# Kernel optimization log

Measured on AMD Instinct MI355X. Metric: run time of the kernel, lower is better.

The kernel has to match this reference:

```python
import jax, jax.numpy as jnp
import numpy as np

N, E, C, L, OUT = 50000, 600000, 128, 2, 64


def setup_inputs() -> dict:
    key = jax.random.key(0)
    ks = jax.random.split(key, 8)
    s = 1.0 / np.sqrt(C)
    return {
        "x": jax.random.normal(ks[0], (N, C), jnp.float32),
        "edge_index": jax.random.randint(ks[1], (2, E), 0, N, jnp.int64),
        "W_neigh": jax.random.normal(ks[2], (L, C, C), jnp.float32) * s,
        "W_root": jax.random.normal(ks[3], (L, C, C), jnp.float32) * s,
        "b_conv": jnp.zeros((L, C), jnp.float32),
        "ln_gamma": jnp.ones((L, C), jnp.float32),
        "ln_beta": jnp.zeros((L, C), jnp.float32),
        "W_head": jax.random.normal(ks[4], (OUT, C), jnp.float32) * s,
        "b_head": jnp.zeros((OUT,), jnp.float32),
        "num_seed": 1024,
    }


def _layernorm(h, g, b, eps=1e-5):
    mu = jnp.mean(h, axis=-1, keepdims=True)
    var = jnp.mean(jnp.square(h - mu), axis=-1, keepdims=True)
    return (h - mu) * jax.lax.rsqrt(var + eps) * g + b


def reference(x, edge_index, W_neigh, W_root, b_conv, ln_gamma, ln_beta, W_head, b_head, num_seed):
    src, dst = edge_index[0], edge_index[1]
    n = x.shape[0]
    # in-degree for mean aggregation (clamped to 1 as in PyG mean aggr)
    deg = jax.ops.segment_sum(jnp.ones((src.shape[0],), x.dtype), dst, num_segments=n)
    inv_deg = 1.0 / jnp.maximum(deg, 1.0)  # [N]
    for l in range(W_neigh.shape[0]):
        agg = jax.ops.segment_sum(x[src], dst, num_segments=n) * inv_deg[:, None]  # [N,C]
        h = agg @ W_neigh[l].T + x @ W_root[l].T + b_conv[l]
        x = jax.nn.relu(_layernorm(h, ln_gamma[l], ln_beta[l]))
    # head on the seed nodes (entity table slice starts at 0 here)
    return x[:num_seed] @ W_head.T + b_head
```

## Files before the change

### kernel.cpp

```cpp
#include <hip/hip_runtime.h>

#define C 128

typedef __attribute__((ext_vector_type(8))) short short8;
typedef __attribute__((ext_vector_type(16))) float floatx16;

__device__ __forceinline__ unsigned short f2b(float f) {
    union { float f; unsigned u; } v; v.f = f;
    unsigned u = v.u + 0x7fffu + ((v.u >> 16) & 1u);
    return (unsigned short)(u >> 16);
}
__device__ __forceinline__ void acc_pair(unsigned u, float& lo, float& hi) {
    union { unsigned u; float f; } a, b;
    a.u = u << 16;
    b.u = u & 0xffff0000u;
    lo += a.f;
    hi += b.f;
}

__global__ void cast_mark_count_kernel(const float* __restrict__ x, unsigned short* __restrict__ xb, int n4x,
                                       const float* __restrict__ Wn, unsigned short* __restrict__ Wnb,
                                       const float* __restrict__ Wr, unsigned short* __restrict__ Wrb, int n4w,
                                       const float* __restrict__ Wh, unsigned short* __restrict__ Whb, int n4h,
                                       const int* __restrict__ src, const int* __restrict__ dst,
                                       int* __restrict__ deg, int* __restrict__ needed,
                                       int E, int num_seed,
                                       int castBlocks) {
    if ((int)blockIdx.x < castBlocks) {
        int i = blockIdx.x * blockDim.x + threadIdx.x;
        const float* in;
        unsigned short* out;
        int idx;
        if (i < n4x) { in = x; out = xb; idx = i; }
        else if (i < n4x + n4w) { in = Wn; out = Wnb; idx = i - n4x; }
        else if (i < n4x + 2 * n4w) { in = Wr; out = Wrb; idx = i - n4x - n4w; }
        else if (i < n4x + 2 * n4w + n4h) { in = Wh; out = Whb; idx = i - n4x - 2 * n4w; }
        else return;
        float4 v = ((const float4*)in)[idx];
        ushort4 o;
        o.x = f2b(v.x); o.y = f2b(v.y); o.z = f2b(v.z); o.w = f2b(v.w);
        ((ushort4*)out)[idx] = o;
    } else {
        int e = (blockIdx.x - castBlocks) * blockDim.x + threadIdx.x;
        if (e < num_seed) needed[e] = 1;
        if (e < E) {
            int d = dst[e];
            atomicAdd(&deg[d], 1);
            if (d < num_seed) needed[src[e]] = 1;
        }
    }
}

__global__ void scan_fused_kernel(const int* __restrict__ deg, const int* __restrict__ needed,
                                  unsigned long long* __restrict__ status, int* __restrict__ counter,
                                  int* __restrict__ row_start, int* __restrict__ cursor,
                                  int* __restrict__ nodelist, int* __restrict__ Mptr, int n) {
    __shared__ int smD[256];
    __shared__ int smN[256];
    __shared__ int sbid, sprefD, sprefN;
    int t = threadIdx.x;
    if (t == 0) sbid = atomicAdd(counter, 1);
    __syncthreads();
    int bid = sbid;
    int i = bid * 256 + t;
    int d = (i < n) ? deg[i] : 0;
    int nd = (i < n) ? needed[i] : 0;
    smD[t] = d; smN[t] = nd;
    __syncthreads();
    for (int off = 1; off < 256; off <<= 1) {
        int vD = (t >= off) ? smD[t - off] : 0;
        int vN = (t >= off) ? smN[t - off] : 0;
        __syncthreads();
        smD[t] += vD; smN[t] += vN;
        __syncthreads();
    }
    int totD = smD[255], totN = smN[255];
    if (t == 0) {
        if (bid == 0) {
            atomicExch(&status[0],
                       (2ULL << 62) | ((unsigned long long)(unsigned)totN << 32) | (unsigned)totD);
            sprefD = 0; sprefN = 0;
        } else {
            atomicExch(&status[bid],
                       (1ULL << 62) | ((unsigned long long)(unsigned)totN << 32) | (unsigned)totD);
            int accD = 0, accN = 0;
            for (int j = bid - 1; j >= 0;) {
                unsigned long long v = atomicAdd(&status[j], 0ULL);
                unsigned f = (unsigned)(v >> 62);
                if (f == 0) { __builtin_amdgcn_s_sleep(1); continue; }
                accD += (int)(unsigned)(v & 0xffffffffULL);
                accN += (int)((v >> 32) & 0x3fffffffULL);
                if (f == 2) break;
                --j;
            }
            atomicExch(&status[bid],
                       (2ULL << 62) | ((unsigned long long)(unsigned)(accN + totN) << 32) |
                           (unsigned)(accD + totD));
            sprefD = accD; sprefN = accN;
        }
    }
    __syncthreads();
    int exD = smD[t] - d + sprefD;
    int exN = smN[t] - nd + sprefN;
    if (i < n) {
        row_start[i] = exD;
        cursor[i] = exD;
        if (nd) nodelist[exN] = i;
        if (i == n - 1) { row_start[n] = exD + d; *Mptr = exN + nd; }
    }
}

__global__ void bucket_kernel(const int* __restrict__ src, const int* __restrict__ dst,
                              int* __restrict__ cursor, int* __restrict__ esrc, int E,
                              const int* __restrict__ needed) {
    int e = blockIdx.x * blockDim.x + threadIdx.x;
    if (e < E) {
        int d = dst[e];
        if (needed[d]) {
            int p = atomicAdd(&cursor[d], 1);
            esrc[p] = src[e];
        }
    }
}

__launch_bounds__(256)
__global__ void gemm_fused_kernel(const unsigned short* __restrict__ cur,
                                  const int* __restrict__ row_start, const int* __restrict__ esrc,
                                  const unsigned short* __restrict__ Wn,
                                  const unsigned short* __restrict__ Wr,
                                  const float* __restrict__ bconv, const float* __restrict__ gamma,
                                  const float* __restrict__ beta, unsigned short* __restrict__ Xout,
                                  int n,
                                  const int* __restrict__ nodelist, const int* __restrict__ Mptr,
                                  const unsigned short* __restrict__ Whb,
                                  const float* __restrict__ bh, float* __restrict__ out) {
    __shared__ unsigned short Xs[64][136];
    __shared__ unsigned short Ws[128][136];
    __shared__ float Ls[64][2];
    __shared__ float Lss[64][2];

    int m = Mptr ? *Mptr : n;
    int row0 = blockIdx.x * 64;
    if (row0 >= m) return;

    int tid = threadIdx.x;
    int wave = tid >> 6, lane = tid & 63;
    int rh = wave & 1, ch = wave >> 1;
    int l31 = lane & 31, half = lane >> 5;

#pragma unroll
    for (int i = 0; i < 8; ++i) {
        int cidx = tid + 256 * i;
        int r = cidx >> 4, koff = (cidx & 15) * 8;
        *(uint4*)&Ws[r][koff] = *(const uint4*)(Wn + (size_t)r * C + koff);
    }

    int q = lane >> 4, l16 = lane & 15, qb = lane & 48;
    size_t choff = (size_t)l16 * 8;
#pragma unroll
    for (int pass = 0; pass < 4; ++pass) {
        int rl = pass * 16 + wave * 4 + q;
        int rg = row0 + rl;
        float a0 = 0.f, a1 = 0.f, a2 = 0.f, a3 = 0.f, a4 = 0.f, a5 = 0.f, a6 = 0.f, a7 = 0.f;
        float sc = 0.f;
        if (rg < m) {
            int node = nodelist ? nodelist[rg] : rg;
            int beg = row_start[node];
            int end = row_start[node + 1];
            for (int base = beg; base < end; base += 16) {
                int cnt = min(end - base, 16);
                int e_val = (base + l16 < end) ? esrc[base + l16] : 0;
                int j = 0;
                for (; j + 8 <= cnt; j += 8) {
                    int s0 = __shfl(e_val, qb | j, 64);
                    int s1 = __shfl(e_val, qb | (j + 1), 64);
                    int s2 = __shfl(e_val, qb | (j + 2), 64);
                    int s3 = __shfl(e_val, qb | (j + 3), 64);
                    int s4 = __shfl(e_val, qb | (j + 4), 64);
                    int s5 = __shfl(e_val, qb | (j + 5), 64);
                    int s6 = __shfl(e_val, qb | (j + 6), 64);
                    int s7 = __shfl(e_val, qb | (j + 7), 64);
                    uint4 v0 = *(const uint4*)(cur + (size_t)s0 * C + choff);
                    uint4 v1 = *(const uint4*)(cur + (size_t)s1 * C + choff);
                    uint4 v2 = *(const uint4*)(cur + (size_t)s2 * C + choff);
                    uint4 v3 = *(const uint4*)(cur + (size_t)s3 * C + choff);
                    uint4 v4 = *(const uint4*)(cur + (size_t)s4 * C + choff);
                    uint4 v5 = *(const uint4*)(cur + (size_t)s5 * C + choff);
                    uint4 v6 = *(const uint4*)(cur + (size_t)s6 * C + choff);
                    uint4 v7 = *(const uint4*)(cur + (size_t)s7 * C + choff);
                    acc_pair(v0.x, a0, a1); acc_pair(v0.y, a2, a3); acc_pair(v0.z, a4, a5); acc_pair(v0.w, a6, a7);
                    acc_pair(v1.x, a0, a1); acc_pair(v1.y, a2, a3); acc_pair(v1.z, a4, a5); acc_pair(v1.w, a6, a7);
                    acc_pair(v2.x, a0, a1); acc_pair(v2.y, a2, a3); acc_pair(v2.z, a4, a5); acc_pair(v2.w, a6, a7);
                    acc_pair(v3.x, a0, a1); acc_pair(v3.y, a2, a3); acc_pair(v3.z, a4, a5); acc_pair(v3.w, a6, a7);
                    acc_pair(v4.x, a0, a1); acc_pair(v4.y, a2, a3); acc_pair(v4.z, a4, a5); acc_pair(v4.w, a6, a7);
                    acc_pair(v5.x, a0, a1); acc_pair(v5.y, a2, a3); acc_pair(v5.z, a4, a5); acc_pair(v5.w, a6, a7);
                    acc_pair(v6.x, a0, a1); acc_pair(v6.y, a2, a3); acc_pair(v6.z, a4, a5); acc_pair(v6.w, a6, a7);
                    acc_pair(v7.x, a0, a1); acc_pair(v7.y, a2, a3); acc_pair(v7.z, a4, a5); acc_pair(v7.w, a6, a7);
                }
                for (; j + 4 <= cnt; j += 4) {
                    int s0 = __shfl(e_val, qb | j, 64);
                    int s1 = __shfl(e_val, qb | (j + 1), 64);
                    int s2 = __shfl(e_val, qb | (j + 2), 64);
                    int s3 = __shfl(e_val, qb | (j + 3), 64);
                    uint4 v0 = *(const uint4*)(cur + (size_t)s0 * C + choff);
                    uint4 v1 = *(const uint4*)(cur + (size_t)s1 * C + choff);
                    uint4 v2 = *(const uint4*)(cur + (size_t)s2 * C + choff);
                    uint4 v3 = *(const uint4*)(cur + (size_t)s3 * C + choff);
                    acc_pair(v0.x, a0, a1); acc_pair(v0.y, a2, a3); acc_pair(v0.z, a4, a5); acc_pair(v0.w, a6, a7);
                    acc_pair(v1.x, a0, a1); acc_pair(v1.y, a2, a3); acc_pair(v1.z, a4, a5); acc_pair(v1.w, a6, a7);
                    acc_pair(v2.x, a0, a1); acc_pair(v2.y, a2, a3); acc_pair(v2.z, a4, a5); acc_pair(v2.w, a6, a7);
                    acc_pair(v3.x, a0, a1); acc_pair(v3.y, a2, a3); acc_pair(v3.z, a4, a5); acc_pair(v3.w, a6, a7);
                }
                for (; j < cnt; ++j) {
                    int s0 = __shfl(e_val, qb | j, 64);
                    uint4 v0 = *(const uint4*)(cur + (size_t)s0 * C + choff);
                    acc_pair(v0.x, a0, a1); acc_pair(v0.y, a2, a3); acc_pair(v0.z, a4, a5); acc_pair(v0.w, a6, a7);
                }
            }
            sc = 1.0f / fmaxf((float)(end - beg), 1.0f);
        }
        uint4 o;
        o.x = ((unsigned)f2b(a1 * sc) << 16) | (unsigned)f2b(a0 * sc);
        o.y = ((unsigned)f2b(a3 * sc) << 16) | (unsigned)f2b(a2 * sc);
        o.z = ((unsigned)f2b(a5 * sc) << 16) | (unsigned)f2b(a4 * sc);
        o.w = ((unsigned)f2b(a7 * sc) << 16) | (unsigned)f2b(a6 * sc);
        *(uint4*)&Xs[rl][choff] = o;
    }
    __syncthreads();

    floatx16 acc0, acc1;
#pragma unroll
    for (int i = 0; i < 16; ++i) { acc0[i] = 0.f; acc1[i] = 0.f; }

#pragma unroll
    for (int kc = 0; kc < C; kc += 16) {
        int ko = kc + half * 8;
        short8 a = *(const short8*)&Xs[rh * 32 + l31][ko];
        short8 b0 = *(const short8*)&Ws[ch * 64 + l31][ko];
        short8 b1 = *(const short8*)&Ws[ch * 64 + 32 + l31][ko];
        acc0 = __builtin_amdgcn_mfma_f32_32x32x16_bf16(a, b0, acc0, 0, 0, 0);
        acc1 = __builtin_amdgcn_mfma_f32_32x32x16_bf16(a, b1, acc1, 0, 0, 0);
    }
    __syncthreads();

#pragma unroll
    for (int i = 0; i < 4; ++i) {
        int cidx = tid + 256 * i;
        int r = cidx >> 4, koff = (cidx & 15) * 8;
        uint4 v = make_uint4(0u, 0u, 0u, 0u);
        int rg = row0 + r;
        if (rg < m) {
            int rowid = nodelist ? nodelist[rg] : rg;
            v = *(const uint4*)(cur + (size_t)rowid * C + koff);
        }
        *(uint4*)&Xs[r][koff] = v;
    }
#pragma unroll
    for (int i = 0; i < 8; ++i) {
        int cidx = tid + 256 * i;
        int r = cidx >> 4, koff = (cidx & 15) * 8;
        *(uint4*)&Ws[r][koff] = *(const uint4*)(Wr + (size_t)r * C + koff);
    }
    __syncthreads();

#pragma unroll
    for (int kc = 0; kc < C; kc += 16) {
        int ko = kc + half * 8;
        short8 a = *(const short8*)&Xs[rh * 32 + l31][ko];
        short8 b0 = *(const short8*)&Ws[ch * 64 + l31][ko];
        short8 b1 = *(const short8*)&Ws[ch * 64 + 32 + l31][ko];
        acc0 = __builtin_amdgcn_mfma_f32_32x32x16_bf16(a, b0, acc0, 0, 0, 0);
        acc1 = __builtin_amdgcn_mfma_f32_32x32x16_bf16(a, b1, acc1, 0, 0, 0);
    }

    int col0 = ch * 64 + l31;
    int col1 = col0 + 32;
    float bc0 = bconv[col0], bc1 = bconv[col1];
#pragma unroll
    for (int r = 0; r < 16; ++r) {
        float h0 = acc0[r] + bc0;
        float h1 = acc1[r] + bc1;
        float s = h0 + h1, ss = h0 * h0 + h1 * h1;
#pragma unroll
        for (int mk = 1; mk < 32; mk <<= 1) {
            s += __shfl_xor(s, mk, 64);
            ss += __shfl_xor(ss, mk, 64);
        }
        if (l31 == 0) {
            int row_l = rh * 32 + (r & 3) + 8 * (r >> 2) + 4 * half;
            Ls[row_l][ch] = s;
            Lss[row_l][ch] = ss;
        }
    }
    __syncthreads();

    if (Whb) {
#pragma unroll
        for (int i = 0; i < 4; ++i) {
            int cidx = tid + 256 * i;
            int r = cidx >> 4, koff = (cidx & 15) * 8;
            uint4 v = *(const uint4*)(Whb + (size_t)r * C + koff);
            *(uint4*)&Ws[r][koff] = v;
        }
    }

    float g0 = gamma[col0], g1 = gamma[col1];
    float be0 = beta[col0], be1 = beta[col1];
#pragma unroll
    for (int r = 0; r < 16; ++r) {
        int row_l = rh * 32 + (r & 3) + 8 * (r >> 2) + 4 * half;
        int rg = row0 + row_l;
        float s = Ls[row_l][0] + Ls[row_l][1];
        float ss = Lss[row_l][0] + Lss[row_l][1];
        float mu = s * (1.0f / 128.0f);
        float var = ss * (1.0f / 128.0f) - mu * mu;
        float rs = rsqrtf(var + 1e-5f);
        float h0 = acc0[r] + bc0;
        float h1 = acc1[r] + bc1;
        float o0 = fmaxf((h0 - mu) * rs * g0 + be0, 0.f);
        float o1 = fmaxf((h1 - mu) * rs * g1 + be1, 0.f);
        if (Whb) {
            Xs[row_l][col0] = f2b(o0);
            Xs[row_l][col1] = f2b(o1);
        } else if (rg < m) {
            int orow = nodelist ? nodelist[rg] : rg;
            Xout[(size_t)orow * C + col0] = f2b(o0);
            Xout[(size_t)orow * C + col1] = f2b(o1);
        }
    }

    if (Whb) {
        __syncthreads();
        floatx16 hc;
#pragma unroll
        for (int i = 0; i < 16; ++i) hc[i] = 0.f;
        int m0 = rh * 32, n0 = ch * 32;
#pragma unroll
        for (int kc = 0; kc < C; kc += 16) {
            int ko = kc + half * 8;
            short8 a = *(const short8*)&Xs[m0 + l31][ko];
            short8 b = *(const short8*)&Ws[n0 + l31][ko];
            hc = __builtin_amdgcn_mfma_f32_32x32x16_bf16(a, b, hc, 0, 0, 0);
        }
        int oc = n0 + l31;
        float bhv = bh[oc];
#pragma unroll
        for (int r = 0; r < 16; ++r) {
            int row_l = m0 + (r & 3) + 8 * (r >> 2) + 4 * half;
            int rg = row0 + row_l;
            if (rg < m) out[(size_t)rg * 64 + oc] = hc[r] + bhv;
        }
    }
}

extern "C" void kernel_launch(void* const* d_in, const int* in_sizes, int n_in,
                              void* d_out, int out_size, void* d_ws, size_t ws_size,
                              hipStream_t stream) {
    const float* x = (const float*)d_in[0];
    const int* ei = (const int*)d_in[1];
    const float* Wn = (const float*)d_in[2];
    const float* Wr = (const float*)d_in[3];
    const float* bconv = (const float*)d_in[4];
    const float* gamma = (const float*)d_in[5];
    const float* beta = (const float*)d_in[6];
    const float* Wh = (const float*)d_in[7];
    const float* bh = (const float*)d_in[8];

    int N = in_sizes[0] / C;
    int E = in_sizes[1] / 2;
    int L = in_sizes[2] / (C * C);
    int num_seed = out_size / 64;
    int nchunks = (N + 255) / 256;

    char* ws = (char*)d_ws;
    size_t off = 0;
    auto alloc = [&](size_t bytes) {
        void* p = ws + off;
        off = (off + bytes + 255) & ~(size_t)255;
        return p;
    };
    int* deg = (int*)alloc((size_t)N * 4);
    int* needed = (int*)alloc((size_t)N * 4);
    int* counter = (int*)alloc(256);
    unsigned long long* status = (unsigned long long*)alloc((size_t)nchunks * 8);
    size_t zero_span = off;
    int* row_start = (int*)alloc((size_t)(N + 1) * 4);
    int* cursor = (int*)alloc((size_t)N * 4);
    int* nodelist = (int*)alloc((size_t)N * 4);
    int* Mptr = (int*)alloc(4);
    int* esrc = (int*)alloc((size_t)E * 4);
    unsigned short* xb = (unsigned short*)alloc((size_t)N * C * 2);
    unsigned short* xA = (unsigned short*)alloc((size_t)N * C * 2);
    unsigned short* xB = (unsigned short*)alloc((size_t)N * C * 2);
    unsigned short* Wnb = (unsigned short*)alloc((size_t)L * C * C * 2);
    unsigned short* Wrb = (unsigned short*)alloc((size_t)L * C * C * 2);
    unsigned short* Whb = (unsigned short*)alloc((size_t)64 * C * 2);

    const int* srcIdx = ei;
    const int* dstIdx = ei + E;

    int n4x = N * C / 4;
    int n4w = L * C * C / 4;
    int n4h = 64 * C / 4;
    int castBlocks = (n4x + 2 * n4w + n4h + 255) / 256;
    int degBlocks = (max(E, num_seed) + 255) / 256;

    hipMemsetAsync(ws, 0, zero_span, stream);
    cast_mark_count_kernel<<<castBlocks + degBlocks, 256, 0, stream>>>(
        x, xb, n4x, Wn, Wnb, Wr, Wrb, n4w, Wh, Whb, n4h,
        srcIdx, dstIdx, deg, needed, E, num_seed, castBlocks);
    scan_fused_kernel<<<nchunks, 256, 0, stream>>>(deg, needed, status, counter,
                                                   row_start, cursor, nodelist, Mptr, N);
    bucket_kernel<<<(E + 255) / 256, 256, 0, stream>>>(srcIdx, dstIdx, cursor, esrc, E, needed);

    const unsigned short* cur = xb;
    unsigned short* bufs[2] = {xA, xB};
    for (int l = 0; l < L; ++l) {
        bool last = (l == L - 1);
        bool front = !last && (l == L - 2);
        int nl = last ? num_seed : N;
        const int* list = front ? nodelist : nullptr;
        const int* Mp = front ? Mptr : nullptr;
        unsigned short* nxt = bufs[l & 1];
        gemm_fused_kernel<<<(nl + 63) / 64, 256, 0, stream>>>(
            cur, row_start, esrc,
            Wnb + (size_t)l * C * C, Wrb + (size_t)l * C * C,
            bconv + (size_t)l * C, gamma + (size_t)l * C, beta + (size_t)l * C, nxt, nl,
            list, Mp,
            last ? Whb : (const unsigned short*)nullptr, bh, (float*)d_out);
        cur = nxt;
    }
}
```

Measured before the change: 197.9 us.

## Split neighbor aggregation into a separate kernel before the MFMA GEMM

Moves the gather-and-mean neighbor aggregation out of the fused GEMM kernel into its own wave-per-four-nodes kernel, which writes a bf16 aggregate buffer. The GEMM kernel then loads the aggregate and root rows into shared memory in a uniform two-phase loop and stages its output in LDS for coalesced uint4 stores. The aim is higher occupancy and better latency hiding for the irregular gather, and a simpler, lighter GEMM kernel. The cost is an extra launch per layer plus a write and re-read of an N×C bf16 intermediate.

```diff
diff --git a/kernel.cpp b/kernel.cpp
--- a/kernel.cpp
+++ b/kernel.cpp
@@ -123,17 +123,96 @@
     }
 }
 
+__global__ void aggregate_kernel(const unsigned short* __restrict__ xb, const int* __restrict__ row_start,
+                                 const int* __restrict__ esrc,
+                                 unsigned short* __restrict__ agg, int n,
+                                 const int* __restrict__ nodelist, const int* __restrict__ Mptr) {
+    int wid = (blockIdx.x * blockDim.x + threadIdx.x) >> 6;
+    int lane = threadIdx.x & 63;
+    int q = lane >> 4, l16 = lane & 15;
+    int qb = lane & 48;
+    int pos = wid * 4 + q;
+    int m = Mptr ? *Mptr : n;
+    if (pos >= m) return;
+    int node = nodelist ? nodelist[pos] : pos;
+
+    int beg = row_start[node];
+    int end = row_start[node + 1];
+    size_t choff = (size_t)l16 * 8;
+
+    float a0 = 0.f, a1 = 0.f, a2 = 0.f, a3 = 0.f, a4 = 0.f, a5 = 0.f, a6 = 0.f, a7 = 0.f;
+
+    for (int base = beg; base < end; base += 16) {
+        int cnt = min(end - base, 16);
+        int e_val = (base + l16 < end) ? esrc[base + l16] : 0;
+        int j = 0;
+        for (; j + 8 <= cnt; j += 8) {
+            int s0 = __shfl(e_val, qb | j, 64);
+            int s1 = __shfl(e_val, qb | (j + 1), 64);
+            int s2 = __shfl(e_val, qb | (j + 2), 64);
+            int s3 = __shfl(e_val, qb | (j + 3), 64);
+            int s4 = __shfl(e_val, qb | (j + 4), 64);
+            int s5 = __shfl(e_val, qb | (j + 5), 64);
+            int s6 = __shfl(e_val, qb | (j + 6), 64);
+            int s7 = __shfl(e_val, qb | (j + 7), 64);
+            uint4 v0 = *(const uint4*)(xb + (size_t)s0 * C + choff);
+            uint4 v1 = *(const uint4*)(xb + (size_t)s1 * C + choff);
+            uint4 v2 = *(const uint4*)(xb + (size_t)s2 * C + choff);
+            uint4 v3 = *(const uint4*)(xb + (size_t)s3 * C + choff);
+            uint4 v4 = *(const uint4*)(xb + (size_t)s4 * C + choff);
+            uint4 v5 = *(const uint4*)(xb + (size_t)s5 * C + choff);
+            uint4 v6 = *(const uint4*)(xb + (size_t)s6 * C + choff);
+            uint4 v7 = *(const uint4*)(xb + (size_t)s7 * C + choff);
+            acc_pair(v0.x, a0, a1); acc_pair(v0.y, a2, a3); acc_pair(v0.z, a4, a5); acc_pair(v0.w, a6, a7);
+            acc_pair(v1.x, a0, a1); acc_pair(v1.y, a2, a3); acc_pair(v1.z, a4, a5); acc_pair(v1.w, a6, a7);
+            acc_pair(v2.x, a0, a1); acc_pair(v2.y, a2, a3); acc_pair(v2.z, a4, a5); acc_pair(v2.w, a6, a7);
+            acc_pair(v3.x, a0, a1); acc_pair(v3.y, a2, a3); acc_pair(v3.z, a4, a5); acc_pair(v3.w, a6, a7);
+            acc_pair(v4.x, a0, a1); acc_pair(v4.y, a2, a3); acc_pair(v4.z, a4, a5); acc_pair(v4.w, a6, a7);
+            acc_pair(v5.x, a0, a1); acc_pair(v5.y, a2, a3); acc_pair(v5.z, a4, a5); acc_pair(v5.w, a6, a7);
+            acc_pair(v6.x, a0, a1); acc_pair(v6.y, a2, a3); acc_pair(v6.z, a4, a5); acc_pair(v6.w, a6, a7);
+            acc_pair(v7.x, a0, a1); acc_pair(v7.y, a2, a3); acc_pair(v7.z, a4, a5); acc_pair(v7.w, a6, a7);
+        }
+        for (; j + 4 <= cnt; j += 4) {
+            int s0 = __shfl(e_val, qb | j, 64);
+            int s1 = __shfl(e_val, qb | (j + 1), 64);
+            int s2 = __shfl(e_val, qb | (j + 2), 64);
+            int s3 = __shfl(e_val, qb | (j + 3), 64);
+            uint4 v0 = *(const uint4*)(xb + (size_t)s0 * C + choff);
+            uint4 v1 = *(const uint4*)(xb + (size_t)s1 * C + choff);
+            uint4 v2 = *(const uint4*)(xb + (size_t)s2 * C + choff);
+            uint4 v3 = *(const uint4*)(xb + (size_t)s3 * C + choff);
+            acc_pair(v0.x, a0, a1); acc_pair(v0.y, a2, a3); acc_pair(v0.z, a4, a5); acc_pair(v0.w, a6, a7);
+            acc_pair(v1.x, a0, a1); acc_pair(v1.y, a2, a3); acc_pair(v1.z, a4, a5); acc_pair(v1.w, a6, a7);
+            acc_pair(v2.x, a0, a1); acc_pair(v2.y, a2, a3); acc_pair(v2.z, a4, a5); acc_pair(v2.w, a6, a7);
+            acc_pair(v3.x, a0, a1); acc_pair(v3.y, a2, a3); acc_pair(v3.z, a4, a5); acc_pair(v3.w, a6, a7);
+        }
+        for (; j < cnt; ++j) {
+            int s0 = __shfl(e_val, qb | j, 64);
+            uint4 v0 = *(const uint4*)(xb + (size_t)s0 * C + choff);
+            acc_pair(v0.x, a0, a1); acc_pair(v0.y, a2, a3); acc_pair(v0.z, a4, a5); acc_pair(v0.w, a6, a7);
+        }
+    }
+
+    float sc = 1.0f / fmaxf((float)(end - beg), 1.0f);
+    uint4 o;
+    o.x = ((unsigned)f2b(a1 * sc) << 16) | (unsigned)f2b(a0 * sc);
+    o.y = ((unsigned)f2b(a3 * sc) << 16) | (unsigned)f2b(a2 * sc);
+    o.z = ((unsigned)f2b(a5 * sc) << 16) | (unsigned)f2b(a4 * sc);
+    o.w = ((unsigned)f2b(a7 * sc) << 16) | (unsigned)f2b(a6 * sc);
+    *(uint4*)(agg + (size_t)pos * C + choff) = o;
+}
+
 __launch_bounds__(256)
-__global__ void gemm_fused_kernel(const unsigned short* __restrict__ cur,
-                                  const int* __restrict__ row_start, const int* __restrict__ esrc,
-                                  const unsigned short* __restrict__ Wn,
-                                  const unsigned short* __restrict__ Wr,
-                                  const float* __restrict__ bconv, const float* __restrict__ gamma,
-                                  const float* __restrict__ beta, unsigned short* __restrict__ Xout,
-                                  int n,
-                                  const int* __restrict__ nodelist, const int* __restrict__ Mptr,
-                                  const unsigned short* __restrict__ Whb,
-                                  const float* __restrict__ bh, float* __restrict__ out) {
+__global__ void gemm_mfma_ln_relu_kernel(const unsigned short* __restrict__ Aagg,
+                                         const unsigned short* __restrict__ Xin,
+                                         const unsigned short* __restrict__ Wn,
+                                         const unsigned short* __restrict__ Wr,
+                                         const float* __restrict__ bconv, const float* __restrict__ gamma,
+                                         const float* __restrict__ beta, unsigned short* __restrict__ Xout,
+                                         int n,
+                                         const int* __restrict__ nodelist, const int* __restrict__ Mptr,
+                                         const unsigned short* __restrict__ Whb,
+                                         const float* __restrict__ bh, float* __restrict__ out) {
     __shared__ unsigned short Xs[64][136];
     __shared__ unsigned short Ws[128][136];
     __shared__ float Ls[64][2];
@@ -148,129 +227,44 @@
     int rh = wave & 1, ch = wave >> 1;
     int l31 = lane & 31, half = lane >> 5;
 
-#pragma unroll
-    for (int i = 0; i < 8; ++i) {
-        int cidx = tid + 256 * i;
-        int r = cidx >> 4, koff = (cidx & 15) * 8;
-        *(uint4*)&Ws[r][koff] = *(const uint4*)(Wn + (size_t)r * C + koff);
-    }
-
-    int q = lane >> 4, l16 = lane & 15, qb = lane & 48;
-    size_t choff = (size_t)l16 * 8;
-#pragma unroll
-    for (int pass = 0; pass < 4; ++pass) {
-        int rl = pass * 16 + wave * 4 + q;
-        int rg = row0 + rl;
-        float a0 = 0.f, a1 = 0.f, a2 = 0.f, a3 = 0.f, a4 = 0.f, a5 = 0.f, a6 = 0.f, a7 = 0.f;
-        float sc = 0.f;
-        if (rg < m) {
-            int node = nodelist ? nodelist[rg] : rg;
-            int beg = row_start[node];
-            int end = row_start[node + 1];
-            for (int base = beg; base < end; base += 16) {
-                int cnt = min(end - base, 16);
-                int e_val = (base + l16 < end) ? esrc[base + l16] : 0;
-                int j = 0;
-                for (; j + 8 <= cnt; j += 8) {
-                    int s0 = __shfl(e_val, qb | j, 64);
-                    int s1 = __shfl(e_val, qb | (j + 1), 64);
-                    int s2 = __shfl(e_val, qb | (j + 2), 64);
-                    int s3 = __shfl(e_val, qb | (j + 3), 64);
-                    int s4 = __shfl(e_val, qb | (j + 4), 64);
-                    int s5 = __shfl(e_val, qb | (j + 5), 64);
-                    int s6 = __shfl(e_val, qb | (j + 6), 64);
-                    int s7 = __shfl(e_val, qb | (j + 7), 64);
-                    uint4 v0 = *(const uint4*)(cur + (size_t)s0 * C + choff);
-                    uint4 v1 = *(const uint4*)(cur + (size_t)s1 * C + choff);
-                    uint4 v2 = *(const uint4*)(cur + (size_t)s2 * C + choff);
-                    uint4 v3 = *(const uint4*)(cur + (size_t)s3 * C + choff);
-                    uint4 v4 = *(const uint4*)(cur + (size_t)s4 * C + choff);
-                    uint4 v5 = *(const uint4*)(cur + (size_t)s5 * C + choff);
-                    uint4 v6 = *(const uint4*)(cur + (size_t)s6 * C + choff);
-                    uint4 v7 = *(const uint4*)(cur + (size_t)s7 * C + choff);
-                    acc_pair(v0.x, a0, a1); acc_pair(v0.y, a2, a3); acc_pair(v0.z, a4, a5); acc_pair(v0.w, a6, a7);
-                    acc_pair(v1.x, a0, a1); acc_pair(v1.y, a2, a3); acc_pair(v1.z, a4, a5); acc_pair(v1.w, a6, a7);
-                    acc_pair(v2.x, a0, a1); acc_pair(v2.y, a2, a3); acc_pair(v2.z, a4, a5); acc_pair(v2.w, a6, a7);
-                    acc_pair(v3.x, a0, a1); acc_pair(v3.y, a2, a3); acc_pair(v3.z, a4, a5); acc_pair(v3.w, a6, a7);
-                    acc_pair(v4.x, a0, a1); acc_pair(v4.y, a2, a3); acc_pair(v4.z, a4, a5); acc_pair(v4.w, a6, a7);
-                    acc_pair(v5.x, a0, a1); acc_pair(v5.y, a2, a3); acc_pair(v5.z, a4, a5); acc_pair(v5.w, a6, a7);
-                    acc_pair(v6.x, a0, a1); acc_pair(v6.y, a2, a3); acc_pair(v6.z, a4, a5); acc_pair(v6.w, a6, a7);
-                    acc_pair(v7.x, a0, a1); acc_pair(v7.y, a2, a3); acc_pair(v7.z, a4, a5); acc_pair(v7.w, a6, a7);
-                }
-                for (; j + 4 <= cnt; j += 4) {
-                    int s0 = __shfl(e_val, qb | j, 64);
-                    int s1 = __shfl(e_val, qb | (j + 1), 64);
-                    int s2 = __shfl(e_val, qb | (j + 2), 64);
-                    int s3 = __shfl(e_val, qb | (j + 3), 64);
-                    uint4 v0 = *(const uint4*)(cur + (size_t)s0 * C + choff);
-                    uint4 v1 = *(const uint4*)(cur + (size_t)s1 * C + choff);
-                    uint4 v2 = *(const uint4*)(cur + (size_t)s2 * C + choff);
-                    uint4 v3 = *(const uint4*)(cur + (size_t)s3 * C + choff);
-                    acc_pair(v0.x, a0, a1); acc_pair(v0.y, a2, a3); acc_pair(v0.z, a4, a5); acc_pair(v0.w, a6, a7);
-                    acc_pair(v1.x, a0, a1); acc_pair(v1.y, a2, a3); acc_pair(v1.z, a4, a5); acc_pair(v1.w, a6, a7);
-                    acc_pair(v2.x, a0, a1); acc_pair(v2.y, a2, a3); acc_pair(v2.z, a4, a5); acc_pair(v2.w, a6, a7);
-                    acc_pair(v3.x, a0, a1); acc_pair(v3.y, a2, a3); acc_pair(v3.z, a4, a5); acc_pair(v3.w, a6, a7);
-                }
-                for (; j < cnt; ++j) {
-                    int s0 = __shfl(e_val, qb | j, 64);
-                    uint4 v0 = *(const uint4*)(cur + (size_t)s0 * C + choff);
-                    acc_pair(v0.x, a0, a1); acc_pair(v0.y, a2, a3); acc_pair(v0.z, a4, a5); acc_pair(v0.w, a6, a7);
-                }
+    floatx16 acc0, acc1;
+#pragma unroll
+    for (int i = 0; i < 16; ++i) { acc0[i] = 0.f; acc1[i] = 0.f; }
+
+#pragma unroll
+    for (int phase = 0; phase < 2; ++phase) {
+        const unsigned short* Ap = phase ? Xin : Aagg;
+        const unsigned short* Wp = phase ? Wr : Wn;
+        __syncthreads();
+#pragma unroll
+        for (int i = 0; i < 4; ++i) {
+            int cidx = tid + 256 * i;
+            int r = cidx >> 4, koff = (cidx & 15) * 8;
+            uint4 v = make_uint4(0u, 0u, 0u, 0u);
+            int rg = row0 + r;
+            if (rg < m) {
+                int rowid = (phase && nodelist) ? nodelist[rg] : rg;
+                v = *(const uint4*)(Ap + (size_t)rowid * C + koff);
             }
-            sc = 1.0f / fmaxf((float)(end - beg), 1.0f);
-        }
-        uint4 o;
-        o.x = ((unsigned)f2b(a1 * sc) << 16) | (unsigned)f2b(a0 * sc);
-        o.y = ((unsigned)f2b(a3 * sc) << 16) | (unsigned)f2b(a2 * sc);
-        o.z = ((unsigned)f2b(a5 * sc) << 16) | (unsigned)f2b(a4 * sc);
-        o.w = ((unsigned)f2b(a7 * sc) << 16) | (unsigned)f2b(a6 * sc);
-        *(uint4*)&Xs[rl][choff] = o;
-    }
-    __syncthreads();
-
-    floatx16 acc0, acc1;
-#pragma unroll
-    for (int i = 0; i < 16; ++i) { acc0[i] = 0.f; acc1[i] = 0.f; }
-
-#pragma unroll
-    for (int kc = 0; kc < C; kc += 16) {
-        int ko = kc + half * 8;
-        short8 a = *(const short8*)&Xs[rh * 32 + l31][ko];
-        short8 b0 = *(const short8*)&Ws[ch * 64 + l31][ko];
-        short8 b1 = *(const short8*)&Ws[ch * 64 + 32 + l31][ko];
-        acc0 = __builtin_amdgcn_mfma_f32_32x32x16_bf16(a, b0, acc0, 0, 0, 0);
-        acc1 = __builtin_amdgcn_mfma_f32_32x32x16_bf16(a, b1, acc1, 0, 0, 0);
-    }
-    __syncthreads();
-
-#pragma unroll
-    for (int i = 0; i < 4; ++i) {
-        int cidx = tid + 256 * i;
-        int r = cidx >> 4, koff = (cidx & 15) * 8;
-        uint4 v = make_uint4(0u, 0u, 0u, 0u);
-        int rg = row0 + r;
-        if (rg < m) {
-            int rowid = nodelist ? nodelist[rg] : rg;
-            v = *(const uint4*)(cur + (size_t)rowid * C + koff);
-        }
-        *(uint4*)&Xs[r][koff] = v;
-    }
-#pragma unroll
-    for (int i = 0; i < 8; ++i) {
-        int cidx = tid + 256 * i;
-        int r = cidx >> 4, koff = (cidx & 15) * 8;
-        *(uint4*)&Ws[r][koff] = *(const uint4*)(Wr + (size_t)r * C + koff);
-    }
-    __syncthreads();
-
-#pragma unroll
-    for (int kc = 0; kc < C; kc += 16) {
-        int ko = kc + half * 8;
-        short8 a = *(const short8*)&Xs[rh * 32 + l31][ko];
-        short8 b0 = *(const short8*)&Ws[ch * 64 + l31][ko];
-        short8 b1 = *(const short8*)&Ws[ch * 64 + 32 + l31][ko];
-        acc0 = __builtin_amdgcn_mfma_f32_32x32x16_bf16(a, b0, acc0, 0, 0, 0);
-        acc1 = __builtin_amdgcn_mfma_f32_32x32x16_bf16(a, b1, acc1, 0, 0, 0);
+            *(uint4*)&Xs[r][koff] = v;
+        }
+#pragma unroll
+        for (int i = 0; i < 8; ++i) {
+            int cidx = tid + 256 * i;
+            int r = cidx >> 4, koff = (cidx & 15) * 8;
+            uint4 v = *(const uint4*)(Wp + (size_t)r * C + koff);
+            *(uint4*)&Ws[r][koff] = v;
+        }
+        __syncthreads();
+#pragma unroll
+        for (int kc = 0; kc < C; kc += 16) {
+            int ko = kc + half * 8;
+            short8 a = *(const short8*)&Xs[rh * 32 + l31][ko];
+            short8 b0 = *(const short8*)&Ws[ch * 64 + l31][ko];
+            short8 b1 = *(const short8*)&Ws[ch * 64 + 32 + l31][ko];
+            acc0 = __builtin_amdgcn_mfma_f32_32x32x16_bf16(a, b0, acc0, 0, 0, 0);
+            acc1 = __builtin_amdgcn_mfma_f32_32x32x16_bf16(a, b1, acc1, 0, 0, 0);
+        }
     }
 
     int col0 = ch * 64 + l31;
@@ -309,7 +303,6 @@
 #pragma unroll
     for (int r = 0; r < 16; ++r) {
         int row_l = rh * 32 + (r & 3) + 8 * (r >> 2) + 4 * half;
-        int rg = row0 + row_l;
         float s = Ls[row_l][0] + Ls[row_l][1];
         float ss = Lss[row_l][0] + Lss[row_l][1];
         float mu = s * (1.0f / 128.0f);
@@ -319,18 +312,12 @@
         float h1 = acc1[r] + bc1;
         float o0 = fmaxf((h0 - mu) * rs * g0 + be0, 0.f);
         float o1 = fmaxf((h1 - mu) * rs * g1 + be1, 0.f);
-        if (Whb) {
-            Xs[row_l][col0] = f2b(o0);
-            Xs[row_l][col1] = f2b(o1);
-        } else if (rg < m) {
-            int orow = nodelist ? nodelist[rg] : rg;
-            Xout[(size_t)orow * C + col0] = f2b(o0);
-            Xout[(size_t)orow * C + col1] = f2b(o1);
-        }
-    }
+        Xs[row_l][col0] = f2b(o0);
+        Xs[row_l][col1] = f2b(o1);
+    }
+    __syncthreads();
 
     if (Whb) {
-        __syncthreads();
         floatx16 hc;
 #pragma unroll
         for (int i = 0; i < 16; ++i) hc[i] = 0.f;
@@ -349,6 +336,17 @@
             int row_l = m0 + (r & 3) + 8 * (r >> 2) + 4 * half;
             int rg = row0 + row_l;
             if (rg < m) out[(size_t)rg * 64 + oc] = hc[r] + bhv;
+        }
+    } else {
+#pragma unroll
+        for (int i = 0; i < 4; ++i) {
+            int cidx = tid + 256 * i;
+            int r = cidx >> 4, koff = (cidx & 15) * 8;
+            int rg = row0 + r;
+            if (rg < m) {
+                int orow = nodelist ? nodelist[rg] : rg;
+                *(uint4*)(Xout + (size_t)orow * C + koff) = *(const uint4*)&Xs[r][koff];
+            }
         }
     }
 }
@@ -390,6 +388,7 @@
     int* Mptr = (int*)alloc(4);
     int* esrc = (int*)alloc((size_t)E * 4);
     unsigned short* xb = (unsigned short*)alloc((size_t)N * C * 2);
+    unsigned short* aggb = (unsigned short*)alloc((size_t)N * C * 2);
     unsigned short* xA = (unsigned short*)alloc((size_t)N * C * 2);
     unsigned short* xB = (unsigned short*)alloc((size_t)N * C * 2);
     unsigned short* Wnb = (unsigned short*)alloc((size_t)L * C * C * 2);
@@ -422,9 +421,11 @@
         const int* list = front ? nodelist : nullptr;
         const int* Mp = front ? Mptr : nullptr;
         unsigned short* nxt = bufs[l & 1];
-        gemm_fused_kernel<<<(nl + 63) / 64, 256, 0, stream>>>(
-            cur, row_start, esrc,
-            Wnb + (size_t)l * C * C, Wrb + (size_t)l * C * C,
+        int aggThreads = ((nl + 3) / 4) * 64;
+        aggregate_kernel<<<(aggThreads + 255) / 256, 256, 0, stream>>>(
+            cur, row_start, esrc, aggb, nl, list, Mp);
+        gemm_mfma_ln_relu_kernel<<<(nl + 63) / 64, 256, 0, stream>>>(
+            aggb, cur, Wnb + (size_t)l * C * C, Wrb + (size_t)l * C * C,
             bconv + (size_t)l * C, gamma + (size_t)l * C, beta + (size_t)l * C, nxt, nl,
             list, Mp,
             last ? Whb : (const unsigned short*)nullptr, bh, (float*)d_out);
```

New measurement: 181.0 us. 1.09x faster.
